# Optimization experiments

Hardware: AMD Instinct MI355X
Metric: run time of the kernel (lower is better)

The kernel has to match this reference:

```python
import jax, jax.numpy as jnp
import numpy as np

B, C, T, N = 8, 128, 64, 256
D_STATE, D_CONV, EXPAND = 4, 3, 1
D_INNER = EXPAND * C
DT_RANK = (C + 15) // 16  # 8


def setup_inputs() -> dict:
    key = jax.random.key(0)
    ks = jax.random.split(key, 8)
    s = lambda k, shape, sc=0.02: jax.random.normal(k, shape, jnp.float32) * sc
    return {
        "x": jax.random.normal(ks[0], (B, C, T, N), jnp.float32),
        "ln_gamma": jnp.ones((C,), jnp.float32),
        "ln_beta": jnp.zeros((C,), jnp.float32),
        "in_proj_w": s(ks[1], (2 * D_INNER, C)),
        "conv_w": s(ks[2], (D_CONV, 1, D_INNER), 0.1),
        "conv_b": jnp.zeros((D_INNER,), jnp.float32),
        "x_proj_w": s(ks[3], (DT_RANK + 2 * D_STATE, D_INNER)),
        "dt_proj_w": s(ks[4], (D_INNER, DT_RANK), 0.1),
        "dt_proj_b": s(ks[5], (D_INNER,), 0.1),
        "A_log": jnp.log(jnp.broadcast_to(jnp.arange(1, D_STATE + 1, dtype=jnp.float32), (D_INNER, D_STATE))),
        "D": jnp.ones((D_INNER,), jnp.float32),
        "out_proj_w": s(ks[6], (C, D_INNER)),
    }


def _mamba(x, in_proj_w, conv_w, conv_b, x_proj_w, dt_proj_w, dt_proj_b, A_log, D, out_proj_w):
    # x: (BN, T, C) -- selective-scan Mamba block, single (forward) direction
    xz = x @ in_proj_w.T                                   # (BN, T, 2*D_INNER)
    xc, z = jnp.split(xz, 2, axis=-1)
    # causal depthwise conv along time
    xp = jnp.pad(xc, ((0, 0), (D_CONV - 1, 0), (0, 0)))
    xc = jax.lax.conv_general_dilated(
        xp, conv_w, (1,), 'VALID',
        dimension_numbers=('NWC', 'WIO', 'NWC'),
        feature_group_count=D_INNER) + conv_b
    xc = jax.nn.silu(xc)
    x_dbl = xc @ x_proj_w.T                                # (BN, T, DT_RANK + 2*D_STATE)
    dt, Bs, Cs = jnp.split(x_dbl, [DT_RANK, DT_RANK + D_STATE], axis=-1)
    dt = jax.nn.softplus(dt @ dt_proj_w.T + dt_proj_b)     # (BN, T, D_INNER)
    A = -jnp.exp(A_log)                                    # (D_INNER, D_STATE)
    dA = jnp.exp(dt[..., None] * A)                        # (BN, T, D_INNER, D_STATE)
    dBx = dt[..., None] * Bs[:, :, None, :] * xc[..., None]

    def step(h, inps):
        dA_t, dBx_t, C_t = inps
        h = h * dA_t + dBx_t                               # (BN, D_INNER, D_STATE)
        y = jnp.einsum('bdn,bn->bd', h, C_t)
        return h, y

    h0 = jnp.zeros((xc.shape[0], D_INNER, D_STATE), xc.dtype)
    _, ys = jax.lax.scan(step, h0, (dA.transpose(1, 0, 2, 3),
                                    dBx.transpose(1, 0, 2, 3),
                                    Cs.transpose(1, 0, 2)))
    y = ys.transpose(1, 0, 2) + xc * D                     # (BN, T, D_INNER)
    y = y * jax.nn.silu(z)                                 # gate (if_divide_out=False)
    return y @ out_proj_w.T


def reference(x, ln_gamma, ln_beta, in_proj_w, conv_w, conv_b, x_proj_w,
              dt_proj_w, dt_proj_b, A_log, D, out_proj_w):
    # (B, C, T, N) -> (B, T, N, C)
    h = x.transpose(0, 2, 3, 1)
    mu = h.mean(-1, keepdims=True)
    var = h.var(-1, keepdims=True)
    h = (h - mu) / jnp.sqrt(var + 1e-5) * ln_gamma + ln_beta
    h = h.astype(jnp.float32)  # fp32 cast (autocast disabled around mamba)
    bb, tt, nn, cc = h.shape
    # temporal mode: each (batch, node) pair is an independent time sequence
    hs = h.transpose(0, 2, 1, 3).reshape(bb * nn, tt, cc)
    y = _mamba(hs, in_proj_w, conv_w, conv_b, x_proj_w, dt_proj_w, dt_proj_b,
               A_log, D, out_proj_w)
    y = y.reshape(bb, nn, tt, cc).transpose(0, 2, 1, 3)    # (B, T, N, C)
    return y.transpose(0, 3, 1, 2)                         # (B, C, T, N)
```

## Files before the change

### kernel.cpp

```cpp
#include <hip/hip_runtime.h>
#include <math.h>

#define B_   8
#define C_   128
#define T_   64
#define N_   256
#define NSEQ 4

typedef __attribute__((ext_vector_type(8))) short bf16x8;
typedef __attribute__((ext_vector_type(4))) float f32x4;
typedef unsigned short ushort_t;

#define LOG2E 1.4426950408889634f
#define LN2   0.6931471805599453f

#define RH   0
#define RL   4352
#define R0   8704
#define R1   17152
#define RXD  25728
#define LDSW 27008

__device__ __forceinline__ unsigned bfhi(float x) {
  unsigned u = __float_as_uint(x);
  return (u + 0x7FFF + ((u >> 16) & 1)) >> 16;
}
__device__ __forceinline__ unsigned packsplit(float x) {
  unsigned hi = bfhi(x);
  float rem = x - __uint_as_float(hi << 16);
  unsigned lo = bfhi(rem);
  return (hi & 0xFFFFu) | (lo << 16);
}
__device__ __forceinline__ float unpacksplit(unsigned u) {
  return __uint_as_float(u << 16) + __uint_as_float(u & 0xFFFF0000u);
}
__device__ __forceinline__ float fsilu(float v) {
  return v * __builtin_amdgcn_rcpf(1.0f + __builtin_amdgcn_exp2f(-LOG2E * v));
}
__device__ __forceinline__ float qsum4(float v) {
  int x = __builtin_amdgcn_update_dpp(0, __float_as_int(v), 0xB1, 0xF, 0xF, true);
  v += __int_as_float(x);
  x = __builtin_amdgcn_update_dpp(0, __float_as_int(v), 0x4E, 0xF, 0xF, true);
  v += __int_as_float(x);
  return v;
}
template <int SI>
__device__ __forceinline__ float qbcast(float v) {
  constexpr int sel = SI | (SI << 2) | (SI << 4) | (SI << 6);
  return __int_as_float(__builtin_amdgcn_update_dpp(0, __float_as_int(v), sel, 0xF, 0xF, true));
}
__device__ __forceinline__ int sigq(int qk) { return (qk >> 1) | ((qk & 1) << 2); }
__device__ __forceinline__ int kpos(int k, int s) {
  return (k & ~31) + ((((sigq((k >> 2) & 7)) + s) & 7) << 2) + (k & 3);
}
union BU { uint4 q; bf16x8 v; unsigned u[4]; };

__global__ __launch_bounds__(512) void k_wsplit(const float* __restrict__ Win,
                                                const float* __restrict__ Wout,
                                                const float* __restrict__ Wx,
                                                ushort_t* __restrict__ wsi,
                                                ushort_t* __restrict__ wso,
                                                ushort_t* __restrict__ wsx) {
  int idx = blockIdx.x * 512 + threadIdx.x;
  const float* src;
  ushort_t* dst;
  if (idx < 1024) {
    int row = idx >> 2, kc = idx & 3;
    src = Win + row * 128 + kc * 32;
    dst = wsi + (row * 4 + kc) * 64;
  } else if (idx < 1536) {
    int k = idx - 1024;
    int row = k >> 2, kc = k & 3;
    src = Wout + row * 128 + kc * 32;
    dst = wso + (row * 4 + kc) * 64;
  } else if (idx < 1600) {
    int k = idx - 1536;
    int row = k >> 2, kc = k & 3;
    src = Wx + row * 128 + kc * 32;
    dst = wsx + (row * 4 + kc) * 64;
  } else {
    return;
  }
  for (int g = 0; g < 4; ++g) {
    unsigned hw[4], lw[4];
#pragma unroll
    for (int e2 = 0; e2 < 4; ++e2) {
      float x0 = src[g * 8 + 2 * e2], x1 = src[g * 8 + 2 * e2 + 1];
      unsigned p0 = packsplit(x0), p1 = packsplit(x1);
      hw[e2] = (p0 & 0xFFFFu) | (p1 << 16);
      lw[e2] = (p0 >> 16) | (p1 & 0xFFFF0000u);
    }
    *(uint4*)(dst + (g * 2 + 0) * 8) = make_uint4(hw[0], hw[1], hw[2], hw[3]);
    *(uint4*)(dst + (g * 2 + 1) * 8) = make_uint4(lw[0], lw[1], lw[2], lw[3]);
  }
}

__global__ __launch_bounds__(256) void k_ln(const float* __restrict__ x,
                                            const float* __restrict__ gam,
                                            const float* __restrict__ bet,
                                            unsigned* __restrict__ hp) {
  __shared__ float tile[128 * 36];
  __shared__ float ps[8 * 32], pq[8 * 32], mean_s[32], rstd_s[32];
  int bx = blockIdx.x;
  int nt = bx & 7, t = (bx >> 3) & 63, b = bx >> 9;
  int n0 = nt * 32;
  int tid = threadIdx.x;
  const float4* x4 = (const float4*)x;
  for (int it = 0; it < 4; ++it) {
    int idx4 = it * 256 + tid;
    int c = idx4 >> 3, nn4 = idx4 & 7;
    float4 v = x4[((b * C_ + c) * T_ + t) * (N_ / 4) + (n0 >> 2) + nn4];
    *(float4*)&tile[c * 36 + nn4 * 4] = v;
  }
  __syncthreads();
  {
    int nn = tid & 31, cg = tid >> 5;
    float s = 0.f, q = 0.f;
    for (int i = 0; i < 16; ++i) {
      float v = tile[(cg * 16 + i) * 36 + nn];
      s += v; q += v * v;
    }
    ps[cg * 32 + nn] = s; pq[cg * 32 + nn] = q;
  }
  __syncthreads();
  if (tid < 32) {
    float ss = 0.f, qq = 0.f;
    for (int g2 = 0; g2 < 8; ++g2) { ss += ps[g2 * 32 + tid]; qq += pq[g2 * 32 + tid]; }
    float mu = ss * (1.f / 128.f);
    float var = qq * (1.f / 128.f) - mu * mu;
    mean_s[tid] = mu;
    rstd_s[tid] = rsqrtf(var + 1e-5f);
  }
  __syncthreads();
  {
    int c = tid & 127, half = tid >> 7;
    float gm = gam[c], bb = bet[c];
    ushort_t* hp16 = (ushort_t*)hp;
    for (int it = 0; it < 16; ++it) {
      int n = it * 2 + half;
      float v = (tile[c * 36 + n] - mean_s[n]) * rstd_s[n] * gm + bb;
      unsigned h = bfhi(v);
      unsigned l = bfhi(v - __uint_as_float(h << 16));
      size_t sb = (size_t)(b * N_ + n0 + n) * 8192 + t * 64;
      hp16[(sb + (c >> 1)) * 2 + (c & 1)] = (ushort_t)h;
      hp16[(sb + 4096 + (c >> 1)) * 2 + (c & 1)] = (ushort_t)l;
    }
  }
}

__global__ __launch_bounds__(512, 2) void k_mamba(
    unsigned* ws,
    const ushort_t* __restrict__ wsi,
    const ushort_t* __restrict__ wso,
    const ushort_t* __restrict__ wsx,
    const float* __restrict__ convw,
    const float* __restrict__ convb,
    const float* __restrict__ Wdt,
    const float* __restrict__ bdt,
    const float* __restrict__ Alog,
    const float* __restrict__ Dp)
{
  extern __shared__ float L[];
  unsigned* Li = (unsigned*)L;
  ushort_t* Ls = (ushort_t*)L;
  int tid = threadIdx.x;
  int lane = tid & 63;
  int w = tid >> 6;
  int r16 = lane & 15, g = lane >> 4;
  const uint4* wsi4 = (const uint4*)wsi;
  const uint4* wso4 = (const uint4*)wso;
  const uint4* wsx4 = (const uint4*)wsx;

  uint4 wih[2][4], wil[2][4], woh[4], wol[4];
#pragma unroll
  for (int ci = 0; ci < 2; ++ci)
#pragma unroll
    for (int kc = 0; kc < 4; ++kc) {
      int cb = ((w * 32 + ci * 16 + r16) * 4 + kc) * 8 + g * 2;
      wih[ci][kc] = wsi4[cb];
      wil[ci][kc] = wsi4[cb + 1];
    }
#pragma unroll
  for (int kc = 0; kc < 4; ++kc) {
    int cb = ((w * 16 + r16) * 4 + kc) * 8 + g * 2;
    woh[kc] = wso4[cb];
    wol[kc] = wso4[cb + 1];
  }
  int dc = tid & 127, tq = tid >> 7;
  float cw0 = convw[dc], cw1 = convw[128 + dc], cw2 = convw[256 + dc];
  float cbv = convb[dc];
  int ds = tid >> 2, ss = tid & 3;
  float4 wdta = *(const float4*)&Wdt[ds * 8];
  float4 wdtb = *(const float4*)&Wdt[ds * 8 + 4];
  float bd = bdt[ds];
  float As2 = -expf(Alog[ds * 4 + ss]) * LOG2E;
  float Dd = Dp[ds];
  int kc_d = (ds & ~31) + (ds & 3);
  int qs_d = sigq((ds >> 2) & 7);

  for (int iseq = 0; iseq < NSEQ; ++iseq) {
    size_t seqoff = ((size_t)blockIdx.x * NSEQ + iseq) * 8192;

    {
      const uint4* s4 = (const uint4*)(ws + seqoff);
#pragma unroll
      for (int q = 0; q < 4; ++q) {
        int j = q * 512 + tid;
        int plane = j >> 10, jj = j & 1023;
        int row = jj >> 4, c4 = jj & 15;
        uint4 v = s4[j];
        *(uint4*)&Li[(plane ? RL : RH) + row * 68 + c4 * 4] = v;
      }
    }
    __syncthreads();

    f32x4 acc[4][2];
#pragma unroll
    for (int rt = 0; rt < 4; ++rt)
#pragma unroll
      for (int ci = 0; ci < 2; ++ci) acc[rt][ci] = (f32x4){0.f, 0.f, 0.f, 0.f};
#pragma unroll
    for (int kc = 0; kc < 4; ++kc) {
      BU bh0, bl0, bh1, bl1;
      bh0.q = wih[0][kc]; bl0.q = wil[0][kc];
      bh1.q = wih[1][kc]; bl1.q = wil[1][kc];
#pragma unroll
      for (int rt = 0; rt < 4; ++rt) {
        int base = (rt * 16 + r16) * 68 + kc * 16 + g * 4;
        BU ah, al;
        ah.q = *(const uint4*)&Li[RH + base];
        al.q = *(const uint4*)&Li[RL + base];
        acc[rt][0] = __builtin_amdgcn_mfma_f32_16x16x32_bf16(al.v, bh0.v, acc[rt][0], 0, 0, 0);
        acc[rt][0] = __builtin_amdgcn_mfma_f32_16x16x32_bf16(ah.v, bl0.v, acc[rt][0], 0, 0, 0);
        acc[rt][0] = __builtin_amdgcn_mfma_f32_16x16x32_bf16(ah.v, bh0.v, acc[rt][0], 0, 0, 0);
        acc[rt][1] = __builtin_amdgcn_mfma_f32_16x16x32_bf16(al.v, bh1.v, acc[rt][1], 0, 0, 0);
        acc[rt][1] = __builtin_amdgcn_mfma_f32_16x16x32_bf16(ah.v, bl1.v, acc[rt][1], 0, 0, 0);
        acc[rt][1] = __builtin_amdgcn_mfma_f32_16x16x32_bf16(ah.v, bh1.v, acc[rt][1], 0, 0, 0);
      }
    }

    {
      int dl0 = (w & 3) * 32;
      if (w < 4) {
#pragma unroll
        for (int rt = 0; rt < 4; ++rt)
#pragma unroll
          for (int ci = 0; ci < 2; ++ci)
#pragma unroll
            for (int r = 0; r < 4; ++r)
              L[R0 + (rt * 16 + g * 4 + r) * 132 + dl0 + ci * 16 + r16] = acc[rt][ci][r];
      } else {
#pragma unroll
        for (int rt = 0; rt < 4; ++rt)
#pragma unroll
          for (int ci = 0; ci < 2; ++ci)
#pragma unroll
            for (int r = 0; r < 4; ++r)
              L[R1 + (dl0 + ci * 16 + r16) * 67 + rt * 16 + g * 4 + r] = fsilu(acc[rt][ci][r]);
      }
    }
    __syncthreads();

    {
      int t0 = tq * 16;
      float xin[18];
#pragma unroll
      for (int ii = 0; ii < 18; ++ii) {
        int t = t0 - 2 + ii;
        xin[ii] = (t < 0) ? 0.f : L[R0 + t * 132 + dc];
      }
      __syncthreads();
#pragma unroll
      for (int ii = 0; ii < 16; ++ii) {
        int t = t0 + ii;
        float v = fmaf(cw2, xin[ii + 2], fmaf(cw1, xin[ii + 1], fmaf(cw0, xin[ii], cbv)));
        Li[R0 + t * 132 + kpos(dc, t & 7)] = packsplit(fsilu(v));
      }
    }
    __syncthreads();

    if (w < 4) {
      int s = r16 & 7;
      int slotA = (g + s) & 7, slotB = (g + 4 + s) & 7;
      f32x4 o = (f32x4){0.f, 0.f, 0.f, 0.f};
#pragma unroll
      for (int kc = 0; kc < 4; ++kc) {
        int cb = (r16 * 4 + kc) * 8 + g * 2;
        BU bh, bl;
        bh.q = wsx4[cb];
        bl.q = wsx4[cb + 1];
        int base = R0 + (w * 16 + r16) * 132 + kc * 32;
        uint4 wa = *(const uint4*)&Li[base + slotA * 4];
        uint4 wb = *(const uint4*)&Li[base + slotB * 4];
        BU ah, al;
        ah.u[0] = __builtin_amdgcn_perm(wa.y, wa.x, 0x05040100u);
        ah.u[1] = __builtin_amdgcn_perm(wa.w, wa.z, 0x05040100u);
        ah.u[2] = __builtin_amdgcn_perm(wb.y, wb.x, 0x05040100u);
        ah.u[3] = __builtin_amdgcn_perm(wb.w, wb.z, 0x05040100u);
        al.u[0] = __builtin_amdgcn_perm(wa.y, wa.x, 0x07060302u);
        al.u[1] = __builtin_amdgcn_perm(wa.w, wa.z, 0x07060302u);
        al.u[2] = __builtin_amdgcn_perm(wb.y, wb.x, 0x07060302u);
        al.u[3] = __builtin_amdgcn_perm(wb.w, wb.z, 0x07060302u);
        o = __builtin_amdgcn_mfma_f32_16x16x32_bf16(al.v, bh.v, o, 0, 0, 0);
        o = __builtin_amdgcn_mfma_f32_16x16x32_bf16(ah.v, bl.v, o, 0, 0, 0);
        o = __builtin_amdgcn_mfma_f32_16x16x32_bf16(ah.v, bh.v, o, 0, 0, 0);
      }
      int p = (r16 < 8) ? r16 : (r16 < 12 ? 8 + 2 * (r16 - 8) : 9 + 2 * (r16 - 12));
#pragma unroll
      for (int q = 0; q < 4; ++q)
        L[RXD + (w * 16 + g * 4 + q) * 20 + p] = o[q];
    }
    __syncthreads();

    {
      float hsv = 0.f;
#pragma unroll 4
      for (int tb = 0; tb < 16; ++tb) {
        int tme = tb * 4 + ss;
        const float* xr = &L[RXD + tme * 20];
        float4 xa = *(const float4*)xr;
        float4 xb = *(const float4*)(xr + 4);
        float dot = bd;
        dot = fmaf(xa.x, wdta.x, dot); dot = fmaf(xa.y, wdta.y, dot);
        dot = fmaf(xa.z, wdta.z, dot); dot = fmaf(xa.w, wdta.w, dot);
        dot = fmaf(xb.x, wdtb.x, dot); dot = fmaf(xb.y, wdtb.y, dot);
        dot = fmaf(xb.z, wdtb.z, dot); dot = fmaf(xb.w, wdtb.w, dot);
        float e = __builtin_amdgcn_exp2f(dot * LOG2E);
        float sp = LN2 * __builtin_amdgcn_logf(1.0f + e);
        float dtme = (dot > 20.f) ? dot : sp;

#define SCANSTEP(SI)                                                          \
        {                                                                     \
          int t = tb * 4 + SI;                                                \
          float dtv = qbcast<SI>(dtme);                                       \
          float2 bc = *(const float2*)&L[RXD + t * 20 + 8 + 2 * ss];          \
          int xoff = R0 + t * 132 + kc_d + (((qs_d + (t & 7)) & 7) << 2);     \
          float xcv = unpacksplit(Li[xoff]);                                  \
          float dA = __builtin_amdgcn_exp2f(dtv * As2);                       \
          hsv = fmaf(hsv, dA, dtv * xcv * bc.x);                              \
          float y = qsum4(hsv * bc.y);                                        \
          if (SI == ss) {                                                     \
            y = fmaf(xcv, Dd, y);                                             \
            y *= L[R1 + ds * 67 + t];                                         \
            unsigned yh = bfhi(y);                                            \
            unsigned yl = bfhi(y - __uint_as_float(yh << 16));                \
            int wi = t * 68 + (ds >> 1);                                      \
            Ls[(RH + wi) * 2 + (ds & 1)] = (ushort_t)yh;                      \
            Ls[(RL + wi) * 2 + (ds & 1)] = (ushort_t)yl;                      \
          }                                                                   \
        }
        SCANSTEP(0)
        SCANSTEP(1)
        SCANSTEP(2)
        SCANSTEP(3)
#undef SCANSTEP
      }
    }
    __syncthreads();

    {
      f32x4 o[4];
#pragma unroll
      for (int rt = 0; rt < 4; ++rt) o[rt] = (f32x4){0.f, 0.f, 0.f, 0.f};
#pragma unroll
      for (int kc = 0; kc < 4; ++kc) {
        BU bh, bl;
        bh.q = woh[kc];
        bl.q = wol[kc];
#pragma unroll
        for (int rt = 0; rt < 4; ++rt) {
          int base = (rt * 16 + r16) * 68 + kc * 16 + g * 4;
          BU ah, al;
          ah.q = *(const uint4*)&Li[RH + base];
          al.q = *(const uint4*)&Li[RL + base];
          o[rt] = __builtin_amdgcn_mfma_f32_16x16x32_bf16(al.v, bh.v, o[rt], 0, 0, 0);
          o[rt] = __builtin_amdgcn_mfma_f32_16x16x32_bf16(ah.v, bl.v, o[rt], 0, 0, 0);
          o[rt] = __builtin_amdgcn_mfma_f32_16x16x32_bf16(ah.v, bh.v, o[rt], 0, 0, 0);
        }
      }
      float* yout = (float*)(ws + seqoff);
#pragma unroll
      for (int rt = 0; rt < 4; ++rt)
#pragma unroll
        for (int r = 0; r < 4; ++r)
          yout[(rt * 16 + g * 4 + r) * C_ + w * 16 + r16] = o[rt][r];
    }
    __syncthreads();
  }
}

__global__ __launch_bounds__(256) void k_out_tr(const float* __restrict__ ws_y,
                                                float* __restrict__ out) {
  __shared__ float tile[32 * 132];
  int bx = blockIdx.x;
  int nt = bx & 7, t = (bx >> 3) & 63, b = bx >> 9;
  int n0 = nt * 32;
  int tid = threadIdx.x;
  const float4* y4 = (const float4*)ws_y;
  for (int it = 0; it < 4; ++it) {
    int idx4 = it * 256 + tid;
    int nn = idx4 >> 5, c4 = idx4 & 31;
    float4 v = y4[((b * N_ + n0 + nn) * (long)T_ + t) * (C_ / 4) + c4];
    *(float4*)&tile[nn * 132 + c4 * 4] = v;
  }
  __syncthreads();
  int nn = tid & 31, cg = tid >> 5;
  for (int i = 0; i < 16; ++i) {
    int c = cg * 16 + i;
    out[((b * C_ + c) * (long)T_ + t) * N_ + n0 + nn] = tile[nn * 132 + c];
  }
}

extern "C" void kernel_launch(void* const* d_in, const int* in_sizes, int n_in,
                              void* d_out, int out_size, void* d_ws, size_t ws_size,
                              hipStream_t stream) {
  const float* x    = (const float*)d_in[0];
  const float* gam  = (const float*)d_in[1];
  const float* bet  = (const float*)d_in[2];
  const float* Win  = (const float*)d_in[3];
  const float* cw   = (const float*)d_in[4];
  const float* cb   = (const float*)d_in[5];
  const float* Wx   = (const float*)d_in[6];
  const float* Wdt  = (const float*)d_in[7];
  const float* bdt  = (const float*)d_in[8];
  const float* Alog = (const float*)d_in[9];
  const float* Dp   = (const float*)d_in[10];
  const float* Wout = (const float*)d_in[11];
  float* out = (float*)d_out;
  unsigned* ws = (unsigned*)d_ws;

  const size_t HBYTES = 67108864ull;
  const size_t WBYTES = 131072ull + 65536ull + 8192ull;
  char* wtail;
  if (ws_size >= HBYTES + WBYTES) wtail = (char*)d_ws + HBYTES;
  else                            wtail = (char*)d_out;
  ushort_t* wsi = (ushort_t*)wtail;
  ushort_t* wso = (ushort_t*)(wtail + 131072);
  ushort_t* wsx = (ushort_t*)(wtail + 131072 + 65536);

  (void)hipFuncSetAttribute((const void*)k_mamba,
                            hipFuncAttributeMaxDynamicSharedMemorySize,
                            LDSW * 4);

  k_wsplit<<<4, 512, 0, stream>>>(Win, Wout, Wx, wsi, wso, wsx);
  k_ln<<<4096, 256, 0, stream>>>(x, gam, bet, ws);
  k_mamba<<<2048 / NSEQ, 512, LDSW * 4, stream>>>(ws, wsi, wso, wsx, cw, cb,
                                                  Wdt, bdt, Alog, Dp);
  k_out_tr<<<4096, 256, 0, stream>>>((const float*)ws, out);
}
```

Baseline: 212.4 us.

## Prefetch next sequence into registers, add conv output buffer, hoist scan LDS loads

Each block now handles 8 sequences instead of 4, which halves the grid. The next sequence's input is prefetched from global memory into registers while the current MFMA work runs, so load latency is hidden. The conv output goes to a new LDS region (RXC), which removes one __syncthreads. The scan loop loads its B/C, x and gate values for all 4 substeps up front. This raises LDS use and register pressure, and the smaller grid may lower occupancy or leave CUs idle.

```diff
diff --git a/kernel.cpp b/kernel.cpp
--- a/kernel.cpp
+++ b/kernel.cpp
@@ -5,7 +5,7 @@
 #define C_   128
 #define T_   64
 #define N_   256
-#define NSEQ 4
+#define NSEQ 8
 
 typedef __attribute__((ext_vector_type(8))) short bf16x8;
 typedef __attribute__((ext_vector_type(4))) float f32x4;
@@ -19,7 +19,8 @@
 #define R0   8704
 #define R1   17152
 #define RXD  25728
-#define LDSW 27008
+#define RXC  27008
+#define LDSW 35456
 
 __device__ __forceinline__ unsigned bfhi(float x) {
   unsigned u = __float_as_uint(x);
@@ -198,19 +199,22 @@
   int kc_d = (ds & ~31) + (ds & 3);
   int qs_d = sigq((ds >> 2) & 7);
 
+  uint4 pf[4];
+  {
+    const uint4* s4 = (const uint4*)(ws + (size_t)blockIdx.x * NSEQ * 8192);
+#pragma unroll
+    for (int q = 0; q < 4; ++q) pf[q] = s4[q * 512 + tid];
+  }
+
   for (int iseq = 0; iseq < NSEQ; ++iseq) {
     size_t seqoff = ((size_t)blockIdx.x * NSEQ + iseq) * 8192;
 
-    {
-      const uint4* s4 = (const uint4*)(ws + seqoff);
-#pragma unroll
-      for (int q = 0; q < 4; ++q) {
-        int j = q * 512 + tid;
-        int plane = j >> 10, jj = j & 1023;
-        int row = jj >> 4, c4 = jj & 15;
-        uint4 v = s4[j];
-        *(uint4*)&Li[(plane ? RL : RH) + row * 68 + c4 * 4] = v;
-      }
+#pragma unroll
+    for (int q = 0; q < 4; ++q) {
+      int j = q * 512 + tid;
+      int plane = j >> 10, jj = j & 1023;
+      int row = jj >> 4, c4 = jj & 15;
+      *(uint4*)&Li[(plane ? RL : RH) + row * 68 + c4 * 4] = pf[q];
     }
     __syncthreads();
 
@@ -238,6 +242,11 @@
         acc[rt][1] = __builtin_amdgcn_mfma_f32_16x16x32_bf16(ah.v, bh1.v, acc[rt][1], 0, 0, 0);
       }
     }
+    if (iseq + 1 < NSEQ) {
+      const uint4* s4n = (const uint4*)(ws + seqoff + 8192);
+#pragma unroll
+      for (int q = 0; q < 4; ++q) pf[q] = s4n[q * 512 + tid];
+    }
 
     {
       int dl0 = (w & 3) * 32;
@@ -269,12 +278,11 @@
         int t = t0 - 2 + ii;
         xin[ii] = (t < 0) ? 0.f : L[R0 + t * 132 + dc];
       }
-      __syncthreads();
 #pragma unroll
       for (int ii = 0; ii < 16; ++ii) {
         int t = t0 + ii;
         float v = fmaf(cw2, xin[ii + 2], fmaf(cw1, xin[ii + 1], fmaf(cw0, xin[ii], cbv)));
-        Li[R0 + t * 132 + kpos(dc, t & 7)] = packsplit(fsilu(v));
+        Li[RXC + t * 132 + kpos(dc, t & 7)] = packsplit(fsilu(v));
       }
     }
     __syncthreads();
@@ -289,7 +297,7 @@
         BU bh, bl;
         bh.q = wsx4[cb];
         bl.q = wsx4[cb + 1];
-        int base = R0 + (w * 16 + r16) * 132 + kc * 32;
+        int base = RXC + (w * 16 + r16) * 132 + kc * 32;
         uint4 wa = *(const uint4*)&Li[base + slotA * 4];
         uint4 wb = *(const uint4*)&Li[base + slotB * 4];
         BU ah, al;
@@ -320,6 +328,15 @@
         const float* xr = &L[RXD + tme * 20];
         float4 xa = *(const float4*)xr;
         float4 xb = *(const float4*)(xr + 4);
+        float zg = L[R1 + ds * 67 + tme];
+        float2 bc[4];
+        unsigned xu[4];
+#pragma unroll
+        for (int si = 0; si < 4; ++si) {
+          int t = tb * 4 + si;
+          bc[si] = *(const float2*)&L[RXD + t * 20 + 8 + 2 * ss];
+          xu[si] = Li[RXC + t * 132 + kc_d + (((qs_d + (t & 7)) & 7) << 2)];
+        }
         float dot = bd;
         dot = fmaf(xa.x, wdta.x, dot); dot = fmaf(xa.y, wdta.y, dot);
         dot = fmaf(xa.z, wdta.z, dot); dot = fmaf(xa.w, wdta.w, dot);
@@ -328,23 +345,20 @@
         float e = __builtin_amdgcn_exp2f(dot * LOG2E);
         float sp = LN2 * __builtin_amdgcn_logf(1.0f + e);
         float dtme = (dot > 20.f) ? dot : sp;
+        int wi = tme * 68 + (ds >> 1);
 
 #define SCANSTEP(SI)                                                          \
         {                                                                     \
-          int t = tb * 4 + SI;                                                \
           float dtv = qbcast<SI>(dtme);                                       \
-          float2 bc = *(const float2*)&L[RXD + t * 20 + 8 + 2 * ss];          \
-          int xoff = R0 + t * 132 + kc_d + (((qs_d + (t & 7)) & 7) << 2);     \
-          float xcv = unpacksplit(Li[xoff]);                                  \
+          float xcv = unpacksplit(xu[SI]);                                    \
           float dA = __builtin_amdgcn_exp2f(dtv * As2);                       \
-          hsv = fmaf(hsv, dA, dtv * xcv * bc.x);                              \
-          float y = qsum4(hsv * bc.y);                                        \
+          hsv = fmaf(hsv, dA, dtv * xcv * bc[SI].x);                          \
+          float y = qsum4(hsv * bc[SI].y);                                    \
           if (SI == ss) {                                                     \
             y = fmaf(xcv, Dd, y);                                             \
-            y *= L[R1 + ds * 67 + t];                                         \
+            y *= zg;                                                          \
             unsigned yh = bfhi(y);                                            \
             unsigned yl = bfhi(y - __uint_as_float(yh << 16));                \
-            int wi = t * 68 + (ds >> 1);                                      \
             Ls[(RH + wi) * 2 + (ds & 1)] = (ushort_t)yh;                      \
             Ls[(RL + wi) * 2 + (ds & 1)] = (ushort_t)yl;                      \
           }                                                                   \
```

After: 195.1 us. -8.2%, faster.
